# Kernel optimization log

Measured on AMD Instinct MI355X. Metric: run time of the kernel, lower is better.

## Reference

```python
import jax, jax.numpy as jnp
import numpy as np

B, T, F, H, C = 1048576, 11, 3, 11, 7


def setup_inputs() -> dict:
    key = jax.random.key(0)
    ks = jax.random.split(key, 5)
    x = jax.random.normal(ks[0], (B, T, F), dtype=jnp.float32)
    # GRU params (glorot-ish scale); bias is [2, 3H]: row0=input bias, row1=recurrent bias (reset_after=True)
    kernel = jax.random.normal(ks[1], (F, 3 * H), dtype=jnp.float32) * 0.4
    rec_kernel = jax.random.normal(ks[2], (H, 3 * H), dtype=jnp.float32) * 0.2
    bias = jnp.zeros((2, 3 * H), dtype=jnp.float32)
    dense_w = jax.random.normal(ks[3], (T * H, C), dtype=jnp.float32) * 0.1
    dense_b = jnp.zeros((C,), dtype=jnp.float32)
    return {"x": x, "kernel": kernel, "rec_kernel": rec_kernel, "bias": bias,
            "dense_w": dense_w, "dense_b": dense_b}


def _gru(x, kernel, rec_kernel, bias):
    # Keras GRUCell, reset_after=True, inference (no dropout).
    in_b, rec_b = bias[0], bias[1]
    xm = x @ kernel + in_b  # [B,T,3H] precompute input projections

    def step(h, xt):
        inner = h @ rec_kernel + rec_b  # [B,3H]
        xz, xr, xh = jnp.split(xt, 3, axis=-1)
        rz, rr, rh = jnp.split(inner, 3, axis=-1)
        z = jax.nn.sigmoid(xz + rz)
        r = jax.nn.sigmoid(xr + rr)
        hh = jnp.tanh(xh + r * rh)
        h_new = z * h + (1.0 - z) * hh
        return h_new, h_new

    h0 = jnp.zeros((x.shape[0], rec_kernel.shape[0]), x.dtype)
    _, hs = jax.lax.scan(step, h0, jnp.swapaxes(xm, 0, 1))  # [T,B,H]
    return jnp.swapaxes(hs, 0, 1)  # [B,T,H]


def reference(x, kernel, rec_kernel, bias, dense_w, dense_b):
    hs = _gru(x, kernel, rec_kernel, bias)          # [B,T,H]
    flat = hs.reshape(hs.shape[0], -1)              # [B,T*H]
    logits = flat @ dense_w + dense_b               # [B,C]
    return jax.nn.softmax(logits, axis=-1)
```

## Files before the change

kernel.cpp:

```cpp
#include <hip/hip_runtime.h>

#define TT 11
#define FF 3
#define HH 11
#define CC 7
#define TF 33
#define GBLOCK 512
#define PBLOCK 256
#define L2E 1.44269504088896340736f

typedef _Float16 h4 __attribute__((ext_vector_type(4)));
typedef float f4 __attribute__((ext_vector_type(4)));
typedef unsigned int u2 __attribute__((ext_vector_type(2)));

#define WS_GA 0
#define WS_DA 512
#define WS_TOT 1920

__device__ __forceinline__ float gate_val(int g, int k, int n,
        const float* rk, const float* kk, const float* bias) {
    if (n >= HH) return 0.0f;
    if (g == 0 || g == 1) {
        const int col = (g == 0 ? 0 : HH) + n;
        if (k < HH) return rk[k * TF + col];
        if (k < 14) return kk[(k - 11) * TF + col];
        if (k == 14) return bias[col] + bias[TF + col];
        return 0.0f;
    }
    const int col = 2 * HH + n;
    if (g == 2) {
        if (k < HH) return rk[k * TF + col];
        if (k == 14) return bias[TF + col];
        return 0.0f;
    }
    if (k >= 11 && k < 14) return kk[(k - 11) * TF + col];
    if (k == 14) return bias[col];
    return 0.0f;
}

__global__ void prep_weights(const float* __restrict__ k,
                             const float* __restrict__ rk,
                             const float* __restrict__ bias,
                             const float* __restrict__ dw,
                             const float* __restrict__ db,
                             float* __restrict__ ws) {
    const int tid = threadIdx.x;
    unsigned int* wsu = (unsigned int*)ws;
    if (tid < 256) {
        const int g = tid >> 6, l = tid & 63;
        const int n = l & 15, kb = 4 * (l >> 4);
        const float scale = (g < 2) ? -L2E : (-2.0f * L2E);
        unsigned short h[4];
        #pragma unroll
        for (int i = 0; i < 4; ++i) {
            const float v = gate_val(g, kb + i, n, rk, k, bias) * scale;
            h[i] = __builtin_bit_cast(unsigned short, (_Float16)v);
        }
        wsu[WS_GA + (g * 64 + l) * 2]     = h[0] | ((unsigned int)h[1] << 16);
        wsu[WS_GA + (g * 64 + l) * 2 + 1] = h[2] | ((unsigned int)h[3] << 16);
    }
    for (int idx = tid; idx < TT * 64; idx += PBLOCK) {
        const int t = idx >> 6, l = idx & 63;
        const int c = l & 15, kb = 4 * (l >> 4);
        unsigned short h[4];
        #pragma unroll
        for (int i = 0; i < 4; ++i) {
            const int kk2 = kb + i;
            float v = 0.0f;
            if (c < CC) {
                if (kk2 < HH) v = dw[(t * HH + kk2) * CC + c];
                else if (kk2 == 14 && t == 0) v = db[c];
            }
            h[i] = __builtin_bit_cast(unsigned short, (_Float16)v);
        }
        wsu[WS_DA + idx * 2]     = h[0] | ((unsigned int)h[1] << 16);
        wsu[WS_DA + idx * 2 + 1] = h[2] | ((unsigned int)h[3] << 16);
    }
}

__device__ __forceinline__ unsigned int pkf16(float a, float b) {
    return (unsigned int)__builtin_bit_cast(unsigned short, (_Float16)a) |
           ((unsigned int)__builtin_bit_cast(unsigned short, (_Float16)b) << 16);
}

__global__ __launch_bounds__(GBLOCK, 4) void gru_main(
    const float* __restrict__ x,
    const float* __restrict__ ws,
    float* __restrict__ out,
    int Bt)
{
    __shared__ unsigned int   sxA[GBLOCK * TT];
    __shared__ unsigned short sxB[GBLOCK * TT];
    __shared__ float sda[TT * 128];
    const int tid = threadIdx.x;
    const long long base = (long long)blockIdx.x * GBLOCK;

    for (int i = tid; i < TT * 128; i += GBLOCK) sda[i] = ws[WS_DA + i];

    const int lane = tid & 63, wave = tid >> 6;
    const h4* gfp = (const h4*)ws;
    const h4 Az  = gfp[lane];
    const h4 Ar  = gfp[64 + lane];
    const h4 Arh = gfp[128 + lane];
    const h4 Axh = gfp[192 + lane];

    {
        const long long gbase = base * TF;
        const long long gmax = (long long)Bt * TF;
        unsigned short* sxA16 = (unsigned short*)sxA;
        #pragma unroll
        for (int i = 0; i < TF; ++i) {
            const int e = tid + i * GBLOCK;
            const long long g = gbase + e;
            const float v = (g < gmax) ? x[g] : 0.0f;
            const int b = e / TF, r = e % TF;
            const int t = r / FF, s = r % FF;
            const unsigned short hv = __builtin_bit_cast(unsigned short, (_Float16)v);
            if (s == 0) sxB[b * TT + t] = hv;
            else        sxA16[(b * TT + t) * 2 + (s - 1)] = hv;
        }
    }
    __syncthreads();

    const int q = lane & 15, p = lane >> 4;

    float hD[4][4];
    f4 dC[4];
    #pragma unroll
    for (int k2 = 0; k2 < 4; ++k2) {
        dC[k2] = (f4){0.f, 0.f, 0.f, 0.f};
        #pragma unroll
        for (int r = 0; r < 4; ++r) hD[k2][r] = 0.0f;
    }

    const int ibq = (wave * 64 + q) * TT;
    const f4 zf4 = {0.f, 0.f, 0.f, 0.f};

    #pragma unroll 1
    for (int t = 0; t < TT + 1; ++t) {
        const int tx = (t < TT) ? t : (TT - 1);
        h4 Bv[4];
        #pragma unroll
        for (int k2 = 0; k2 < 4; ++k2) {
            const int xi = ibq + k2 * (16 * TT) + tx;
            unsigned int xw0 = 0u;
            unsigned int xw1 = (p == 3) ? 0x00003C00u : 0u;
            if (p == 3)      xw0 = sxA[xi];
            else if (p == 2) xw1 = ((unsigned int)sxB[xi]) << 16;
            const unsigned int b0 = pkf16(hD[k2][0], hD[k2][1]) | xw0;
            const unsigned int b1 = pkf16(hD[k2][2], hD[k2][3]) | xw1;
            const u2 bb = {b0, b1};
            Bv[k2] = __builtin_bit_cast(h4, bb);
        }
        if (t) {
            const h4 dA = *(const h4*)(sda + (t - 1) * 128 + lane * 2);
            #pragma unroll
            for (int k2 = 0; k2 < 4; ++k2)
                dC[k2] = __builtin_amdgcn_mfma_f32_16x16x16f16(dA, Bv[k2], dC[k2], 0, 0, 0);
        }
        if (t < TT) {
            #pragma unroll
            for (int k2 = 0; k2 < 4; ++k2) {
                f4 vz  = __builtin_amdgcn_mfma_f32_16x16x16f16(Az,  Bv[k2], zf4, 0, 0, 0);
                f4 vv  = __builtin_amdgcn_mfma_f32_16x16x16f16(Ar,  Bv[k2], zf4, 0, 0, 0);
                f4 vrh = __builtin_amdgcn_mfma_f32_16x16x16f16(Arh, Bv[k2], zf4, 0, 0, 0);
                f4 vxh = __builtin_amdgcn_mfma_f32_16x16x16f16(Axh, Bv[k2], zf4, 0, 0, 0);
                #pragma unroll
                for (int r = 0; r < 4; ++r) {
                    const float tz = __builtin_amdgcn_exp2f(vz[r]);
                    const float tv = __builtin_amdgcn_exp2f(vv[r]);
                    const float rr = __builtin_amdgcn_rcpf(1.0f + tv);
                    const float tu = __builtin_amdgcn_exp2f(fmaf(rr, vrh[r], vxh[r]));
                    const float hp = hD[k2][r];
                    const float num = fmaf(tu, hp - tz, hp + tz);
                    const float den = (1.0f + tz) * (1.0f + tu);
                    hD[k2][r] = num * __builtin_amdgcn_rcpf(den);
                }
            }
        }
    }

    __syncthreads();
    float* sf = (float*)sxA;
    #pragma unroll
    for (int k2 = 0; k2 < 4; ++k2) {
        const float d0 = dC[k2][0], d1 = dC[k2][1], d2 = dC[k2][2], d3 = dC[k2][3];
        float mloc = fmaxf(fmaxf(d0, d1), d2);
        if (p == 0) mloc = fmaxf(mloc, d3);
        const float m = fmaxf(mloc, __shfl_xor(mloc, 16, 64));
        const float e0 = __builtin_amdgcn_exp2f((d0 - m) * L2E);
        const float e1 = __builtin_amdgcn_exp2f((d1 - m) * L2E);
        const float e2 = __builtin_amdgcn_exp2f((d2 - m) * L2E);
        const float e3 = (p == 0) ? __builtin_amdgcn_exp2f((d3 - m) * L2E) : 0.0f;
        const float sl = e0 + e1 + e2 + e3;
        const float ssum = sl + __shfl_xor(sl, 16, 64);
        const float inv = __builtin_amdgcn_rcpf(ssum);
        if (p < 2) {
            const int bL = wave * 64 + k2 * 16 + q;
            float* dst = sf + bL * CC + p * 4;
            dst[0] = e0 * inv; dst[1] = e1 * inv; dst[2] = e2 * inv;
            if (p == 0) dst[3] = e3 * inv;
        }
    }
    __syncthreads();
    {
        const long long obase = base * CC;
        const long long omax = (long long)Bt * CC;
        #pragma unroll
        for (int i = 0; i < CC; ++i) {
            const long long g = obase + tid + i * GBLOCK;
            if (g < omax) out[g] = sf[tid + i * GBLOCK];
        }
    }
}

extern "C" void kernel_launch(void* const* d_in, const int* in_sizes, int n_in,
                              void* d_out, int out_size, void* d_ws, size_t ws_size,
                              hipStream_t stream) {
    const float* x  = (const float*)d_in[0];
    const float* k  = (const float*)d_in[1];
    const float* rk = (const float*)d_in[2];
    const float* bi = (const float*)d_in[3];
    const float* dw = (const float*)d_in[4];
    const float* db = (const float*)d_in[5];
    float* out = (float*)d_out;
    float* ws  = (float*)d_ws;

    const int Bt = in_sizes[0] / TF;
    prep_weights<<<1, PBLOCK, 0, stream>>>(k, rk, bi, dw, db, ws);
    const int grid = (Bt + GBLOCK - 1) / GBLOCK;
    gru_main<<<grid, GBLOCK, 0, stream>>>(x, ws, out, Bt);
}
```

Measured before the change: 341.9 us.

## Process 128 batch rows per wave with 256-thread blocks and interleaved MFMA

New measurement: 367.2 us. +7.4%, slower.

```diff
diff --git a/kernel.cpp b/kernel.cpp
--- a/kernel.cpp
+++ b/kernel.cpp
@@ -5,7 +5,9 @@
 #define HH 11
 #define CC 7
 #define TF 33
-#define GBLOCK 512
+#define GBLOCK 256
+#define NK2 8
+#define BPB 512
 #define PBLOCK 256
 #define L2E 1.44269504088896340736f
 
@@ -89,11 +91,11 @@
     float* __restrict__ out,
     int Bt)
 {
-    __shared__ unsigned int   sxA[GBLOCK * TT];
-    __shared__ unsigned short sxB[GBLOCK * TT];
+    __shared__ unsigned int   sxA[BPB * TT];
+    __shared__ unsigned short sxB[BPB * TT];
     __shared__ float sda[TT * 128];
     const int tid = threadIdx.x;
-    const long long base = (long long)blockIdx.x * GBLOCK;
+    const long long base = (long long)blockIdx.x * BPB;
 
     for (int i = tid; i < TT * 128; i += GBLOCK) sda[i] = ws[WS_DA + i];
 
@@ -108,8 +110,7 @@
         const long long gbase = base * TF;
         const long long gmax = (long long)Bt * TF;
         unsigned short* sxA16 = (unsigned short*)sxA;
-        #pragma unroll
-        for (int i = 0; i < TF; ++i) {
+        for (int i = 0; i < BPB * TF / GBLOCK; ++i) {
             const int e = tid + i * GBLOCK;
             const long long g = gbase + e;
             const float v = (g < gmax) ? x[g] : 0.0f;
@@ -124,24 +125,25 @@
 
     const int q = lane & 15, p = lane >> 4;
 
-    float hD[4][4];
-    f4 dC[4];
+    float hD[NK2][4];
+    f4 dC[NK2];
     #pragma unroll
-    for (int k2 = 0; k2 < 4; ++k2) {
+    for (int k2 = 0; k2 < NK2; ++k2) {
         dC[k2] = (f4){0.f, 0.f, 0.f, 0.f};
         #pragma unroll
         for (int r = 0; r < 4; ++r) hD[k2][r] = 0.0f;
     }
 
-    const int ibq = (wave * 64 + q) * TT;
+    const int ibq = (wave * 128 + q) * TT;
     const f4 zf4 = {0.f, 0.f, 0.f, 0.f};
 
     #pragma unroll 1
     for (int t = 0; t < TT + 1; ++t) {
         const int tx = (t < TT) ? t : (TT - 1);
-        h4 Bv[4];
-        #pragma unroll
-        for (int k2 = 0; k2 < 4; ++k2) {
+        h4 dA = {};
+        if (t) dA = *(const h4*)(sda + (t - 1) * 128 + lane * 2);
+        #pragma unroll
+        for (int k2 = 0; k2 < NK2; ++k2) {
             const int xi = ibq + k2 * (16 * TT) + tx;
             unsigned int xw0 = 0u;
             unsigned int xw1 = (p == 3) ? 0x00003C00u : 0u;
@@ -150,21 +152,15 @@
             const unsigned int b0 = pkf16(hD[k2][0], hD[k2][1]) | xw0;
             const unsigned int b1 = pkf16(hD[k2][2], hD[k2][3]) | xw1;
             const u2 bb = {b0, b1};
-            Bv[k2] = __builtin_bit_cast(h4, bb);
-        }
-        if (t) {
-            const h4 dA = *(const h4*)(sda + (t - 1) * 128 + lane * 2);
-            #pragma unroll
-            for (int k2 = 0; k2 < 4; ++k2)
-                dC[k2] = __builtin_amdgcn_mfma_f32_16x16x16f16(dA, Bv[k2], dC[k2], 0, 0, 0);
-        }
-        if (t < TT) {
-            #pragma unroll
-            for (int k2 = 0; k2 < 4; ++k2) {
-                f4 vz  = __builtin_amdgcn_mfma_f32_16x16x16f16(Az,  Bv[k2], zf4, 0, 0, 0);
-                f4 vv  = __builtin_amdgcn_mfma_f32_16x16x16f16(Ar,  Bv[k2], zf4, 0, 0, 0);
-                f4 vrh = __builtin_amdgcn_mfma_f32_16x16x16f16(Arh, Bv[k2], zf4, 0, 0, 0);
-                f4 vxh = __builtin_amdgcn_mfma_f32_16x16x16f16(Axh, Bv[k2], zf4, 0, 0, 0);
+            const h4 Bv = __builtin_bit_cast(h4, bb);
+
+            if (t) dC[k2] = __builtin_amdgcn_mfma_f32_16x16x16f16(dA, Bv, dC[k2], 0, 0, 0);
+
+            if (t < TT) {
+                f4 vz  = __builtin_amdgcn_mfma_f32_16x16x16f16(Az,  Bv, zf4, 0, 0, 0);
+                f4 vv  = __builtin_amdgcn_mfma_f32_16x16x16f16(Ar,  Bv, zf4, 0, 0, 0);
+                f4 vrh = __builtin_amdgcn_mfma_f32_16x16x16f16(Arh, Bv, zf4, 0, 0, 0);
+                f4 vxh = __builtin_amdgcn_mfma_f32_16x16x16f16(Axh, Bv, zf4, 0, 0, 0);
                 #pragma unroll
                 for (int r = 0; r < 4; ++r) {
                     const float tz = __builtin_amdgcn_exp2f(vz[r]);
@@ -173,7 +169,8 @@
                     const float tu = __builtin_amdgcn_exp2f(fmaf(rr, vrh[r], vxh[r]));
                     const float hp = hD[k2][r];
                     const float num = fmaf(tu, hp - tz, hp + tz);
-                    const float den = (1.0f + tz) * (1.0f + tu);
+                    const float d2 = 1.0f + tu;
+                    const float den = fmaf(tz, d2, d2);
                     hD[k2][r] = num * __builtin_amdgcn_rcpf(den);
                 }
             }
@@ -183,7 +180,7 @@
     __syncthreads();
     float* sf = (float*)sxA;
     #pragma unroll
-    for (int k2 = 0; k2 < 4; ++k2) {
+    for (int k2 = 0; k2 < NK2; ++k2) {
         const float d0 = dC[k2][0], d1 = dC[k2][1], d2 = dC[k2][2], d3 = dC[k2][3];
         float mloc = fmaxf(fmaxf(d0, d1), d2);
         if (p == 0) mloc = fmaxf(mloc, d3);
@@ -196,7 +193,7 @@
         const float ssum = sl + __shfl_xor(sl, 16, 64);
         const float inv = __builtin_amdgcn_rcpf(ssum);
         if (p < 2) {
-            const int bL = wave * 64 + k2 * 16 + q;
+            const int bL = wave * 128 + k2 * 16 + q;
             float* dst = sf + bL * CC + p * 4;
             dst[0] = e0 * inv; dst[1] = e1 * inv; dst[2] = e2 * inv;
             if (p == 0) dst[3] = e3 * inv;
@@ -207,7 +204,7 @@
         const long long obase = base * CC;
         const long long omax = (long long)Bt * CC;
         #pragma unroll
-        for (int i = 0; i < CC; ++i) {
+        for (int i = 0; i < BPB * CC / GBLOCK; ++i) {
             const long long g = obase + tid + i * GBLOCK;
             if (g < omax) out[g] = sf[tid + i * GBLOCK];
         }
@@ -228,6 +225,6 @@
 
     const int Bt = in_sizes[0] / TF;
     prep_weights<<<1, PBLOCK, 0, stream>>>(k, rk, bi, dw, db, ws);
-    const int grid = (Bt + GBLOCK - 1) / GBLOCK;
+    const int grid = (Bt + BPB - 1) / BPB;
     gru_main<<<grid, GBLOCK, 0, stream>>>(x, ws, out, Bt);
 }
```
